# Optimization experiments

Measured on AMD Instinct MI355X. Metric: run time of the kernel, lower is better.

Reference implementation:

```python
import jax, jax.numpy as jnp
import numpy as np

E, C, FE, FS, K = 8, 1024, 1024, 4096, 2  # n_experts, embed, expert_inter, shared_inter, top_k
B, T = 4, 2048

def setup_inputs() -> dict:
    key = jax.random.key(0)
    ks = jax.random.split(key, 8)
    def init(k, shape, fan_in):
        return jax.random.normal(k, shape, jnp.float32) / np.sqrt(fan_in).astype(np.float32)
    return dict(
        x=jax.random.normal(ks[0], (B, T, C), jnp.float32),
        gate_w=init(ks[1], (E, C), C),        # nn.Linear(C, E, bias=False).weight
        ew1=init(ks[2], (E, C, FE), C),       # per-expert ln1 weights (transposed)
        ew2=init(ks[3], (E, C, FE), C),       # per-expert ln2 weights
        ewp=init(ks[4], (E, FE, C), FE),      # per-expert proj weights
        sw1=init(ks[5], (C, FS), C),          # shared FFN ln1
        sw2=init(ks[6], (C, FS), C),          # shared FFN ln2
        swp=init(ks[7], (FS, C), FS),         # shared FFN proj
    )

def reference(x, gate_w, ew1, ew2, ewp, sw1, sw2, swp):
    Bd, Td, Cd = x.shape
    xf = x.reshape(-1, Cd)                               # [N, C]
    scores = xf @ gate_w.T                               # [N, E] (eval mode: no noise)
    probs = jax.nn.softmax(scores, axis=-1)
    weights, indices = jax.lax.top_k(probs, K)           # [N, K]
    N = xf.shape[0]
    # combine[n, e] = routing weight of expert e for token n (0 if not selected)
    combine = jnp.zeros((N, E), xf.dtype).at[jnp.arange(N)[:, None], indices].add(weights)
    y = jnp.zeros_like(xf)
    for i in range(E):  # fixed small expert count; masked-dense replaces torch gather/scatter
        h = jax.nn.silu(xf @ ew1[i]) * (xf @ ew2[i])     # [N, FE] SwiGLU
        y = y + (h @ ewp[i]) * combine[:, i:i + 1]
    z = (jax.nn.silu(xf @ sw1) * (xf @ sw2)) @ swp       # shared expert (dropout p=0)
    return (y + z).reshape(Bd, Td, Cd), scores
```

## Files before the change

### kernel.cpp

```cpp
#include <hip/hip_runtime.h>

typedef unsigned short u16;
typedef unsigned int u32;
typedef __bf16 bf16x8 __attribute__((ext_vector_type(8)));
typedef float f32x4 __attribute__((ext_vector_type(4)));
typedef u16 u16x8 __attribute__((ext_vector_type(8)));

#define NTOK 8192
#define CDIM 1024
#define NEXP 8
#define FEDIM 1024
#define FSDIM 4096

#define GLD16(gp, lp) __builtin_amdgcn_global_load_lds( \
    (const __attribute__((address_space(1))) void*)(gp), \
    (__attribute__((address_space(3))) void*)(lp), 16, 0, 0)

__device__ __forceinline__ u16 f2bf(float f) {
  u32 u = __float_as_uint(f);
  u += 0x7FFFu + ((u >> 16) & 1u);
  return (u16)(u >> 16);
}
__device__ __forceinline__ float bf2f(u16 h) {
  return __uint_as_float(((u32)h) << 16);
}

__global__ __launch_bounds__(256) void gate_kernel(
    const float* __restrict__ x, const float* __restrict__ gw,
    float* __restrict__ scores, u16* __restrict__ xb, int* __restrict__ cnt,
    int* __restrict__ tok, float* __restrict__ wgt)
{
  __shared__ int lcnt[NEXP];
  __shared__ int lbase[NEXP];
  __shared__ int rec_i[32];
  __shared__ int rec_p1[32], rec_p2[32];
  __shared__ float rec_w1[32], rec_w2[32];

  int tid = threadIdx.x, wave = tid >> 6, lane = tid & 63;
  if (tid < NEXP) lcnt[tid] = 0;
  __syncthreads();

  int tbase = blockIdx.x * 32 + wave * 8;
#pragma unroll
  for (int it = 0; it < 8; ++it) {
    int n = tbase + it;
    const float4* xr = (const float4*)(x + (size_t)n * CDIM) + lane * 4;
    float4 xv[4];
#pragma unroll
    for (int j = 0; j < 4; j++) xv[j] = xr[j];
    u16x8 rA, rB;
    rA[0]=f2bf(xv[0].x); rA[1]=f2bf(xv[0].y); rA[2]=f2bf(xv[0].z); rA[3]=f2bf(xv[0].w);
    rA[4]=f2bf(xv[1].x); rA[5]=f2bf(xv[1].y); rA[6]=f2bf(xv[1].z); rA[7]=f2bf(xv[1].w);
    rB[0]=f2bf(xv[2].x); rB[1]=f2bf(xv[2].y); rB[2]=f2bf(xv[2].z); rB[3]=f2bf(xv[2].w);
    rB[4]=f2bf(xv[3].x); rB[5]=f2bf(xv[3].y); rB[6]=f2bf(xv[3].z); rB[7]=f2bf(xv[3].w);
    u16* xrow = xb + (size_t)n * CDIM + lane * 16;
    *(u16x8*)xrow = rA;
    *(u16x8*)(xrow + 8) = rB;

    float s[NEXP];
#pragma unroll
    for (int e = 0; e < NEXP; e++) {
      const float4* g = (const float4*)(gw + (size_t)e * CDIM) + lane * 4;
      float a = 0.f;
#pragma unroll
      for (int j = 0; j < 4; j++) {
        float4 gv = g[j];
        a += xv[j].x * gv.x + xv[j].y * gv.y + xv[j].z * gv.z + xv[j].w * gv.w;
      }
#pragma unroll
      for (int o = 32; o > 0; o >>= 1) a += __shfl_xor(a, o);
      s[e] = a;
    }
    if (lane == 0) {
      float m = s[0];
      for (int e = 1; e < NEXP; e++) m = fmaxf(m, s[e]);
      float p[NEXP], sum = 0.f;
      for (int e = 0; e < NEXP; e++) { p[e] = __expf(s[e] - m); sum += p[e]; }
      int i1 = 0;
      for (int e = 1; e < NEXP; e++) if (p[e] > p[i1]) i1 = e;
      int i2 = (i1 == 0) ? 1 : 0;
      for (int e = 0; e < NEXP; e++) if (e != i1 && p[e] > p[i2]) i2 = e;
      float w1 = p[i1] / sum, w2 = p[i2] / sum;
#pragma unroll
      for (int e = 0; e < NEXP; e++) scores[(size_t)n * NEXP + e] = s[e];
      int p1 = atomicAdd(&lcnt[i1], 1);
      int p2 = atomicAdd(&lcnt[i2], 1);
      int slot = wave * 8 + it;
      rec_i[slot] = i1 | (i2 << 8);
      rec_p1[slot] = p1; rec_p2[slot] = p2;
      rec_w1[slot] = w1; rec_w2[slot] = w2;
    }
  }
  __syncthreads();
  if (tid < NEXP) lbase[tid] = atomicAdd(&cnt[tid], lcnt[tid]);
  __syncthreads();
  if (tid < 32) {
    int n = blockIdx.x * 32 + tid;
    int i1 = rec_i[tid] & 0xff, i2 = rec_i[tid] >> 8;
    int q1 = lbase[i1] + rec_p1[tid];
    int q2 = lbase[i2] + rec_p2[tid];
    tok[i1 * NTOK + q1] = n; wgt[i1 * NTOK + q1] = rec_w1[tid];
    tok[i2 * NTOK + q2] = n; wgt[i2 * NTOK + q2] = rec_w2[tid];
  }
}

__global__ __launch_bounds__(256) void transpose64_kernel(
    const float* __restrict__ s0, const float* __restrict__ s1,
    const float* __restrict__ s2, u16* __restrict__ dst,
    int R, int C, int nz_per_src)
{
  __shared__ float tile[64][33];
  int z = blockIdx.z;
  int si = z / nz_per_src;
  const float* src = (si == 0) ? s0 : ((si == 1) ? s1 : s2);
  size_t sbase = (size_t)(z % nz_per_src) * R * C;
  size_t dbase = (size_t)z * R * C;
  int c0 = blockIdx.x * 32, r0 = blockIdx.y * 64;
  int tx = threadIdx.x & 31, ty = threadIdx.x >> 5;
#pragma unroll
  for (int p = 0; p < 8; p++) {
    int r = ty + p * 8;
    tile[r][tx] = src[sbase + (size_t)(r0 + r) * C + c0 + tx];
  }
  __syncthreads();
#pragma unroll
  for (int p = 0; p < 4; p++) {
    int cc = ty + p * 8;
    u32 v = (u32)f2bf(tile[2 * tx][cc]) | ((u32)f2bf(tile[2 * tx + 1][cc]) << 16);
    *(u32*)&dst[dbase + (size_t)(c0 + cc) * R + r0 + 2 * tx] = v;
  }
}

#define BM 128
#define BN 128
#define BK 32
#define TILE (BM * BK)

template<int AMODE>
__global__ __launch_bounds__(256, 2) void gemm_swiglu(
    const u16* __restrict__ A, int lda,
    const u16* __restrict__ B1, const u16* __restrict__ B2,
    size_t bstride, int ldb,
    int M, int K,
    u16* __restrict__ H, int ldh,
    const int* __restrict__ cnt, const int* __restrict__ tok)
{
  int e = blockIdx.z;
  int Mloc = (AMODE == 0) ? M : cnt[e];
  int mbase = blockIdx.y * BM;
  if (AMODE != 0 && mbase >= Mloc) return;
  int nbase = blockIdx.x * BN;
  int tid = threadIdx.x, wid = tid >> 6, lane = tid & 63;

  __shared__ __align__(16) u16 As[2][TILE];
  __shared__ __align__(16) u16 Bs1[2][TILE];
  __shared__ __align__(16) u16 Bs2[2][TILE];

  int sr = lane >> 2;
  int kg = (lane & 3) * 8;
  int arow0 = wid * 32 + sr;
  int arow1 = arow0 + 16;

  int pfx = 0;
  if (AMODE != 0) for (int i = 0; i < NEXP; i++) pfx += (i < e) ? cnt[i] : 0;

  size_t r0, r1;
  if (AMODE == 0) {
    r0 = mbase + arow0; r1 = mbase + arow1;
  } else {
    r0 = tok[e * NTOK + min(mbase + arow0, Mloc - 1)];
    r1 = tok[e * NTOK + min(mbase + arow1, Mloc - 1)];
  }
  const u16* Ap0 = A + r0 * (size_t)lda + kg;
  const u16* Ap1 = A + r1 * (size_t)lda + kg;
  size_t boff = (AMODE != 0) ? (size_t)e * bstride : 0;
  const u16* B1p0 = B1 + boff + (size_t)(nbase + arow0) * ldb + kg;
  const u16* B1p1 = B1 + boff + (size_t)(nbase + arow1) * ldb + kg;
  const u16* B2p0 = B2 + boff + (size_t)(nbase + arow0) * ldb + kg;
  const u16* B2p1 = B2 + boff + (size_t)(nbase + arow1) * ldb + kg;

  int ldsw0 = (wid * 32) * BK;
  int ldsw1 = (wid * 32 + 16) * BK;

  int wr = wid >> 1, wc = wid & 1;
  int fr = lane & 15, fgk = (lane >> 4) * 8;

  f32x4 acc1[4][4] = {};
  f32x4 acc2[4][4] = {};

  int nt = K / BK;
  GLD16(Ap0,  &As [0][ldsw0]); GLD16(Ap1,  &As [0][ldsw1]);
  GLD16(B1p0, &Bs1[0][ldsw0]); GLD16(B1p1, &Bs1[0][ldsw1]);
  GLD16(B2p0, &Bs2[0][ldsw0]); GLD16(B2p1, &Bs2[0][ldsw1]);
  Ap0 += BK; Ap1 += BK; B1p0 += BK; B1p1 += BK; B2p0 += BK; B2p1 += BK;
  __syncthreads();

  int cur = 0;
  for (int t = 0; t < nt; ++t) {
    int nxt = cur ^ 1;
    if (t + 1 < nt) {
      GLD16(Ap0,  &As [nxt][ldsw0]); GLD16(Ap1,  &As [nxt][ldsw1]);
      GLD16(B1p0, &Bs1[nxt][ldsw0]); GLD16(B1p1, &Bs1[nxt][ldsw1]);
      GLD16(B2p0, &Bs2[nxt][ldsw0]); GLD16(B2p1, &Bs2[nxt][ldsw1]);
      Ap0 += BK; Ap1 += BK; B1p0 += BK; B1p1 += BK; B2p0 += BK; B2p1 += BK;
    }
    const u16* as = As[cur];
    const u16* b1s = Bs1[cur];
    const u16* b2s = Bs2[cur];
    bf16x8 af[4], b1f[4], b2f[4];
#pragma unroll
    for (int m = 0; m < 4; m++)
      af[m] = *(const bf16x8*)&as[(wr * 64 + m * 16 + fr) * BK + fgk];
#pragma unroll
    for (int n = 0; n < 4; n++) {
      b1f[n] = *(const bf16x8*)&b1s[(wc * 64 + n * 16 + fr) * BK + fgk];
      b2f[n] = *(const bf16x8*)&b2s[(wc * 64 + n * 16 + fr) * BK + fgk];
    }
#pragma unroll
    for (int m = 0; m < 4; m++)
#pragma unroll
      for (int n = 0; n < 4; n++) {
        acc1[m][n] = __builtin_amdgcn_mfma_f32_16x16x32_bf16(af[m], b1f[n], acc1[m][n], 0, 0, 0);
        acc2[m][n] = __builtin_amdgcn_mfma_f32_16x16x32_bf16(af[m], b2f[n], acc2[m][n], 0, 0, 0);
      }
    __syncthreads();
    cur = nxt;
  }

  int fg4 = (lane >> 4) * 4;
#pragma unroll
  for (int m = 0; m < 4; m++) {
#pragma unroll
    for (int j = 0; j < 4; j++) {
      int rloc = wr * 64 + m * 16 + fg4 + j;
      int rr = mbase + rloc;
      if (AMODE != 0 && rr >= Mloc) continue;
      size_t orow = (size_t)(pfx + rr);
#pragma unroll
      for (int n = 0; n < 4; n++) {
        int col = nbase + wc * 64 + n * 16 + fr;
        float g = acc1[m][n][j];
        float v = acc2[m][n][j];
        float hv = (g / (1.f + __expf(-g))) * v;
        H[orow * (size_t)ldh + col] = f2bf(hv);
      }
    }
  }
}

template<int EPI, int AMODE>
__global__ __launch_bounds__(256, 2) void gemm_proj(
    const u16* __restrict__ A, int lda,
    const u16* __restrict__ B, size_t bstride, int ldb,
    int M, int K,
    float* __restrict__ outF, int ldo,
    const int* __restrict__ cnt, const int* __restrict__ tok,
    const float* __restrict__ wgt)
{
  int e = blockIdx.z;
  int Mloc = (AMODE == 0) ? M : cnt[e];
  int mbase = blockIdx.y * BM;
  if (AMODE != 0 && mbase >= Mloc) return;
  int nbase = blockIdx.x * BN;
  int tid = threadIdx.x, wid = tid >> 6, lane = tid & 63;

  __shared__ __align__(16) u16 As[2][TILE];
  __shared__ __align__(16) u16 Bs[2][TILE];

  int sr = lane >> 2;
  int kg = (lane & 3) * 8;
  int arow0 = wid * 32 + sr;
  int arow1 = arow0 + 16;

  int pfx = 0;
  if (AMODE != 0) for (int i = 0; i < NEXP; i++) pfx += (i < e) ? cnt[i] : 0;

  size_t r0, r1;
  if (AMODE == 0) {
    r0 = mbase + arow0; r1 = mbase + arow1;
  } else {
    r0 = pfx + min(mbase + arow0, Mloc - 1);
    r1 = pfx + min(mbase + arow1, Mloc - 1);
  }
  const u16* Ap0 = A + r0 * (size_t)lda + kg;
  const u16* Ap1 = A + r1 * (size_t)lda + kg;
  const u16* Bb = B + ((AMODE != 0) ? (size_t)e * bstride : 0);
  const u16* Bp0 = Bb + (size_t)(nbase + arow0) * ldb + kg;
  const u16* Bp1 = Bb + (size_t)(nbase + arow1) * ldb + kg;

  int ldsw0 = (wid * 32) * BK;
  int ldsw1 = (wid * 32 + 16) * BK;

  int wr = wid >> 1, wc = wid & 1;
  int fr = lane & 15, fgk = (lane >> 4) * 8;

  f32x4 acc[4][4] = {};

  int nt = K / BK;
  GLD16(Ap0, &As[0][ldsw0]); GLD16(Ap1, &As[0][ldsw1]);
  GLD16(Bp0, &Bs[0][ldsw0]); GLD16(Bp1, &Bs[0][ldsw1]);
  Ap0 += BK; Ap1 += BK; Bp0 += BK; Bp1 += BK;
  __syncthreads();

  int cur = 0;
  for (int t = 0; t < nt; ++t) {
    int nxt = cur ^ 1;
    if (t + 1 < nt) {
      GLD16(Ap0, &As[nxt][ldsw0]); GLD16(Ap1, &As[nxt][ldsw1]);
      GLD16(Bp0, &Bs[nxt][ldsw0]); GLD16(Bp1, &Bs[nxt][ldsw1]);
      Ap0 += BK; Ap1 += BK; Bp0 += BK; Bp1 += BK;
    }
    const u16* as = As[cur];
    const u16* bs = Bs[cur];
    bf16x8 af[4], bfr[4];
#pragma unroll
    for (int m = 0; m < 4; m++)
      af[m] = *(const bf16x8*)&as[(wr * 64 + m * 16 + fr) * BK + fgk];
#pragma unroll
    for (int n = 0; n < 4; n++)
      bfr[n] = *(const bf16x8*)&bs[(wc * 64 + n * 16 + fr) * BK + fgk];
#pragma unroll
    for (int m = 0; m < 4; m++)
#pragma unroll
      for (int n = 0; n < 4; n++)
        acc[m][n] = __builtin_amdgcn_mfma_f32_16x16x32_bf16(af[m], bfr[n], acc[m][n], 0, 0, 0);
    __syncthreads();
    cur = nxt;
  }

  int fg4 = (lane >> 4) * 4;
#pragma unroll
  for (int m = 0; m < 4; m++) {
#pragma unroll
    for (int j = 0; j < 4; j++) {
      int rloc = wr * 64 + m * 16 + fg4 + j;
      int rr = mbase + rloc;
      if (AMODE != 0 && rr >= Mloc) continue;
      int t = 0; float wv = 0.f;
      if (EPI == 4) { t = tok[e * NTOK + rr]; wv = wgt[e * NTOK + rr]; }
#pragma unroll
      for (int n = 0; n < 4; n++) {
        int col = nbase + wc * 64 + n * 16 + fr;
        float v = acc[m][n][j];
        if (EPI == 2) {
          outF[(size_t)rr * ldo + col] = v;
        } else {
          unsafeAtomicAdd(&outF[(size_t)t * ldo + col], v * wv);
        }
      }
    }
  }
}

extern "C" void kernel_launch(void* const* d_in, const int* in_sizes, int n_in,
                              void* d_out, int out_size, void* d_ws, size_t ws_size,
                              hipStream_t stream)
{
  const float* x   = (const float*)d_in[0];
  const float* gw  = (const float*)d_in[1];
  const float* ew1 = (const float*)d_in[2];
  const float* ew2 = (const float*)d_in[3];
  const float* ewp = (const float*)d_in[4];
  const float* sw1 = (const float*)d_in[5];
  const float* sw2 = (const float*)d_in[6];
  const float* swp = (const float*)d_in[7];
  float* out    = (float*)d_out;
  float* scores = out + (size_t)NTOK * CDIM;

  char* wsp = (char*)d_ws;
  size_t off = 0;
  auto alloc = [&](size_t bytes) -> void* {
    void* p = wsp + off; off += (bytes + 255) & ~(size_t)255; return p;
  };
  u16* xb   = (u16*)alloc((size_t)NTOK * CDIM * 2);
  u16* eall = (u16*)alloc((size_t)24 * CDIM * FEDIM * 2);
  u16* ew1t = eall;
  u16* ew2t = eall + (size_t)8 * CDIM * FEDIM;
  u16* ewpt = eall + (size_t)16 * CDIM * FEDIM;
  u16* s12t = (u16*)alloc((size_t)2 * FSDIM * CDIM * 2);
  u16* sw1t = s12t;
  u16* sw2t = s12t + (size_t)FSDIM * CDIM;
  u16* swpt = (u16*)alloc((size_t)CDIM * FSDIM * 2);
  u16* hs   = (u16*)alloc((size_t)NTOK * FSDIM * 2);
  u16* he   = hs;
  int* cnt  = (int*)alloc(256);
  int* tok  = (int*)alloc((size_t)NEXP * NTOK * 4);
  float* wgt = (float*)alloc((size_t)NEXP * NTOK * 4);
  if (off > ws_size) return;

  hipMemsetAsync(cnt, 0, 32, stream);
  gate_kernel<<<NTOK / 32, 256, 0, stream>>>(x, gw, scores, xb, cnt, tok, wgt);

  transpose64_kernel<<<dim3(FEDIM/32, CDIM/64, 24), 256, 0, stream>>>(
      ew1, ew2, ewp, eall, CDIM, FEDIM, 8);
  transpose64_kernel<<<dim3(FSDIM/32, CDIM/64, 2), 256, 0, stream>>>(
      sw1, sw2, sw1, s12t, CDIM, FSDIM, 1);
  transpose64_kernel<<<dim3(CDIM/32, FSDIM/64, 1), 256, 0, stream>>>(
      swp, swp, swp, swpt, FSDIM, CDIM, 1);

  gemm_swiglu<0><<<dim3(FSDIM/BN, NTOK/BM, 1), 256, 0, stream>>>(
      xb, CDIM, sw1t, sw2t, 0, CDIM, NTOK, CDIM, hs, FSDIM, nullptr, nullptr);
  gemm_proj<2,0><<<dim3(CDIM/BN, NTOK/BM, 1), 256, 0, stream>>>(
      hs, FSDIM, swpt, 0, FSDIM, NTOK, FSDIM, out, CDIM, nullptr, nullptr, nullptr);

  size_t estride = (size_t)FEDIM * CDIM;
  gemm_swiglu<1><<<dim3(FEDIM/BN, NTOK/BM, NEXP), 256, 0, stream>>>(
      xb, CDIM, ew1t, ew2t, estride, CDIM, 0, CDIM, he, FEDIM, cnt, tok);
  gemm_proj<4,2><<<dim3(CDIM/BN, NTOK/BM, NEXP), 256, 0, stream>>>(
      he, FEDIM, ewpt, estride, FEDIM, 0, FEDIM, out, CDIM, cnt, tok, wgt);
}
```

Before: 565.1 us.

## Merge gate/transposes, shared+expert SwiGLU, and projections into single launches

Folds the gate kernel and the three weight transposes into one prep kernel, and merges the shared and routed-expert SwiGLU GEMMs into one launch and both projection GEMMs into another, each with a flattened block index. Putting shared and expert work in the same grid lets expert blocks fill the tail of the shared GEMM and removes launch gaps. The shared projection now atomically adds into an output zeroed by a memset instead of storing directly, which adds atomic traffic and a full output memset. The expert hidden buffer gets its own allocation because both GEMMs now run concurrently.

```diff
diff --git a/kernel.cpp b/kernel.cpp
--- a/kernel.cpp
+++ b/kernel.cpp
@@ -21,15 +21,60 @@
   u += 0x7FFFu + ((u >> 16) & 1u);
   return (u16)(u >> 16);
 }
-__device__ __forceinline__ float bf2f(u16 h) {
-  return __uint_as_float(((u32)h) << 16);
-}
-
-__global__ __launch_bounds__(256) void gate_kernel(
+
+__device__ __forceinline__ void transpose64_body(
+    const float* __restrict__ src, u16* __restrict__ dst,
+    int R, int C, int bx, int by)
+{
+  __shared__ float tile[64][33];
+  int c0 = bx * 32, r0 = by * 64;
+  int tx = threadIdx.x & 31, ty = threadIdx.x >> 5;
+#pragma unroll
+  for (int p = 0; p < 8; p++) {
+    int r = ty + p * 8;
+    tile[r][tx] = src[(size_t)(r0 + r) * C + c0 + tx];
+  }
+  __syncthreads();
+#pragma unroll
+  for (int p = 0; p < 4; p++) {
+    int cc = ty + p * 8;
+    u32 v = (u32)f2bf(tile[2 * tx][cc]) | ((u32)f2bf(tile[2 * tx + 1][cc]) << 16);
+    *(u32*)&dst[(size_t)(c0 + cc) * R + r0 + 2 * tx] = v;
+  }
+}
+
+__global__ __launch_bounds__(256) void prep_kernel(
     const float* __restrict__ x, const float* __restrict__ gw,
+    const float* __restrict__ ew1, const float* __restrict__ ew2,
+    const float* __restrict__ ewp, const float* __restrict__ sw1,
+    const float* __restrict__ sw2, const float* __restrict__ swp,
     float* __restrict__ scores, u16* __restrict__ xb, int* __restrict__ cnt,
-    int* __restrict__ tok, float* __restrict__ wgt)
+    int* __restrict__ tok, float* __restrict__ wgt,
+    u16* __restrict__ eall, u16* __restrict__ s12t, u16* __restrict__ swpt)
 {
+  int bid = blockIdx.x;
+  if (bid < 12288) {
+    int z = bid >> 9, r = bid & 511;
+    const float* src = (z < 8) ? ew1 : ((z < 16) ? ew2 : ewp);
+    transpose64_body(src + (size_t)(z & 7) * CDIM * FEDIM,
+                     eall + (size_t)z * CDIM * FEDIM,
+                     CDIM, FEDIM, r & 31, r >> 5);
+    return;
+  }
+  if (bid < 16384) {
+    int i2 = bid - 12288;
+    int z = i2 >> 11, r = i2 & 2047;
+    transpose64_body(z ? sw2 : sw1, s12t + (size_t)z * CDIM * FSDIM,
+                     CDIM, FSDIM, r & 127, r >> 7);
+    return;
+  }
+  if (bid < 18432) {
+    int r = bid - 16384;
+    transpose64_body(swp, swpt, FSDIM, CDIM, r & 31, r >> 5);
+    return;
+  }
+
+  int gb = bid - 18432;
   __shared__ int lcnt[NEXP];
   __shared__ int lbase[NEXP];
   __shared__ int rec_i[32];
@@ -40,7 +85,7 @@
   if (tid < NEXP) lcnt[tid] = 0;
   __syncthreads();
 
-  int tbase = blockIdx.x * 32 + wave * 8;
+  int tbase = gb * 32 + wave * 8;
 #pragma unroll
   for (int it = 0; it < 8; ++it) {
     int n = tbase + it;
@@ -95,7 +140,7 @@
   if (tid < NEXP) lbase[tid] = atomicAdd(&cnt[tid], lcnt[tid]);
   __syncthreads();
   if (tid < 32) {
-    int n = blockIdx.x * 32 + tid;
+    int n = gb * 32 + tid;
     int i1 = rec_i[tid] & 0xff, i2 = rec_i[tid] >> 8;
     int q1 = lbase[i1] + rec_p1[tid];
     int q2 = lbase[i2] + rec_p2[tid];
@@ -104,52 +149,36 @@
   }
 }
 
-__global__ __launch_bounds__(256) void transpose64_kernel(
-    const float* __restrict__ s0, const float* __restrict__ s1,
-    const float* __restrict__ s2, u16* __restrict__ dst,
-    int R, int C, int nz_per_src)
-{
-  __shared__ float tile[64][33];
-  int z = blockIdx.z;
-  int si = z / nz_per_src;
-  const float* src = (si == 0) ? s0 : ((si == 1) ? s1 : s2);
-  size_t sbase = (size_t)(z % nz_per_src) * R * C;
-  size_t dbase = (size_t)z * R * C;
-  int c0 = blockIdx.x * 32, r0 = blockIdx.y * 64;
-  int tx = threadIdx.x & 31, ty = threadIdx.x >> 5;
-#pragma unroll
-  for (int p = 0; p < 8; p++) {
-    int r = ty + p * 8;
-    tile[r][tx] = src[sbase + (size_t)(r0 + r) * C + c0 + tx];
-  }
-  __syncthreads();
-#pragma unroll
-  for (int p = 0; p < 4; p++) {
-    int cc = ty + p * 8;
-    u32 v = (u32)f2bf(tile[2 * tx][cc]) | ((u32)f2bf(tile[2 * tx + 1][cc]) << 16);
-    *(u32*)&dst[dbase + (size_t)(c0 + cc) * R + r0 + 2 * tx] = v;
-  }
-}
-
 #define BM 128
 #define BN 128
 #define BK 32
 #define TILE (BM * BK)
 
-template<int AMODE>
-__global__ __launch_bounds__(256, 2) void gemm_swiglu(
-    const u16* __restrict__ A, int lda,
-    const u16* __restrict__ B1, const u16* __restrict__ B2,
-    size_t bstride, int ldb,
-    int M, int K,
-    u16* __restrict__ H, int ldh,
-    const int* __restrict__ cnt, const int* __restrict__ tok)
+__global__ __launch_bounds__(256, 2) void swiglu_merged(
+    const u16* __restrict__ xb,
+    const u16* __restrict__ sw1t, const u16* __restrict__ sw2t,
+    const u16* __restrict__ ew1t, const u16* __restrict__ ew2t,
+    const int* __restrict__ cnt, const int* __restrict__ tok,
+    u16* __restrict__ hs, u16* __restrict__ he)
 {
-  int e = blockIdx.z;
-  int Mloc = (AMODE == 0) ? M : cnt[e];
-  int mbase = blockIdx.y * BM;
-  if (AMODE != 0 && mbase >= Mloc) return;
-  int nbase = blockIdx.x * BN;
+  int bid = blockIdx.x;
+  bool gather; int e = 0, xB, yB, Mloc, ldh, pfx = 0;
+  const u16 *B1, *B2; u16* H;
+  if (bid < 2048) {
+    gather = false; xB = bid & 31; yB = bid >> 5;
+    Mloc = NTOK; B1 = sw1t; B2 = sw2t; H = hs; ldh = FSDIM;
+  } else {
+    int eb = bid - 2048; e = eb >> 9; int r = eb & 511;
+    xB = r & 7; yB = r >> 3;
+    gather = true;
+    Mloc = cnt[e];
+    if (yB * BM >= Mloc) return;
+    size_t es = (size_t)FEDIM * CDIM;
+    B1 = ew1t + (size_t)e * es; B2 = ew2t + (size_t)e * es;
+    H = he; ldh = FEDIM;
+    for (int i = 0; i < e; i++) pfx += cnt[i];
+  }
+  int mbase = yB * BM, nbase = xB * BN;
   int tid = threadIdx.x, wid = tid >> 6, lane = tid & 63;
 
   __shared__ __align__(16) u16 As[2][TILE];
@@ -161,23 +190,19 @@
   int arow0 = wid * 32 + sr;
   int arow1 = arow0 + 16;
 
-  int pfx = 0;
-  if (AMODE != 0) for (int i = 0; i < NEXP; i++) pfx += (i < e) ? cnt[i] : 0;
-
   size_t r0, r1;
-  if (AMODE == 0) {
+  if (!gather) {
     r0 = mbase + arow0; r1 = mbase + arow1;
   } else {
     r0 = tok[e * NTOK + min(mbase + arow0, Mloc - 1)];
     r1 = tok[e * NTOK + min(mbase + arow1, Mloc - 1)];
   }
-  const u16* Ap0 = A + r0 * (size_t)lda + kg;
-  const u16* Ap1 = A + r1 * (size_t)lda + kg;
-  size_t boff = (AMODE != 0) ? (size_t)e * bstride : 0;
-  const u16* B1p0 = B1 + boff + (size_t)(nbase + arow0) * ldb + kg;
-  const u16* B1p1 = B1 + boff + (size_t)(nbase + arow1) * ldb + kg;
-  const u16* B2p0 = B2 + boff + (size_t)(nbase + arow0) * ldb + kg;
-  const u16* B2p1 = B2 + boff + (size_t)(nbase + arow1) * ldb + kg;
+  const u16* Ap0 = xb + r0 * (size_t)CDIM + kg;
+  const u16* Ap1 = xb + r1 * (size_t)CDIM + kg;
+  const u16* B1p0 = B1 + (size_t)(nbase + arow0) * CDIM + kg;
+  const u16* B1p1 = B1 + (size_t)(nbase + arow1) * CDIM + kg;
+  const u16* B2p0 = B2 + (size_t)(nbase + arow0) * CDIM + kg;
+  const u16* B2p1 = B2 + (size_t)(nbase + arow1) * CDIM + kg;
 
   int ldsw0 = (wid * 32) * BK;
   int ldsw1 = (wid * 32 + 16) * BK;
@@ -188,7 +213,7 @@
   f32x4 acc1[4][4] = {};
   f32x4 acc2[4][4] = {};
 
-  int nt = K / BK;
+  constexpr int nt = CDIM / BK;
   GLD16(Ap0,  &As [0][ldsw0]); GLD16(Ap1,  &As [0][ldsw1]);
   GLD16(B1p0, &Bs1[0][ldsw0]); GLD16(B1p1, &Bs1[0][ldsw1]);
   GLD16(B2p0, &Bs2[0][ldsw0]); GLD16(B2p1, &Bs2[0][ldsw1]);
@@ -234,7 +259,7 @@
     for (int j = 0; j < 4; j++) {
       int rloc = wr * 64 + m * 16 + fg4 + j;
       int rr = mbase + rloc;
-      if (AMODE != 0 && rr >= Mloc) continue;
+      if (gather && rr >= Mloc) continue;
       size_t orow = (size_t)(pfx + rr);
 #pragma unroll
       for (int n = 0; n < 4; n++) {
@@ -248,20 +273,30 @@
   }
 }
 
-template<int EPI, int AMODE>
-__global__ __launch_bounds__(256, 2) void gemm_proj(
-    const u16* __restrict__ A, int lda,
-    const u16* __restrict__ B, size_t bstride, int ldb,
-    int M, int K,
-    float* __restrict__ outF, int ldo,
+__global__ __launch_bounds__(256, 2) void proj_merged(
+    const u16* __restrict__ hs, const u16* __restrict__ he,
+    const u16* __restrict__ swpt, const u16* __restrict__ ewpt,
     const int* __restrict__ cnt, const int* __restrict__ tok,
-    const float* __restrict__ wgt)
+    const float* __restrict__ wgt, float* __restrict__ out)
 {
-  int e = blockIdx.z;
-  int Mloc = (AMODE == 0) ? M : cnt[e];
-  int mbase = blockIdx.y * BM;
-  if (AMODE != 0 && mbase >= Mloc) return;
-  int nbase = blockIdx.x * BN;
+  int bid = blockIdx.x;
+  bool ex; int e = 0, xB, yB, Mloc, K, lda, pfx = 0;
+  const u16 *A, *B;
+  if (bid < 512) {
+    ex = false; xB = bid & 7; yB = bid >> 3;
+    Mloc = NTOK; K = FSDIM; lda = FSDIM; A = hs; B = swpt;
+  } else {
+    int eb = bid - 512; e = eb >> 9; int r = eb & 511;
+    xB = r & 7; yB = r >> 3;
+    ex = true;
+    Mloc = cnt[e];
+    if (yB * BM >= Mloc) return;
+    K = FEDIM; lda = FEDIM; A = he;
+    B = ewpt + (size_t)e * FEDIM * CDIM;
+    for (int i = 0; i < e; i++) pfx += cnt[i];
+  }
+  int mbase = yB * BM, nbase = xB * BN;
+  int ldb = K;
   int tid = threadIdx.x, wid = tid >> 6, lane = tid & 63;
 
   __shared__ __align__(16) u16 As[2][TILE];
@@ -272,11 +307,8 @@
   int arow0 = wid * 32 + sr;
   int arow1 = arow0 + 16;
 
-  int pfx = 0;
-  if (AMODE != 0) for (int i = 0; i < NEXP; i++) pfx += (i < e) ? cnt[i] : 0;
-
   size_t r0, r1;
-  if (AMODE == 0) {
+  if (!ex) {
     r0 = mbase + arow0; r1 = mbase + arow1;
   } else {
     r0 = pfx + min(mbase + arow0, Mloc - 1);
@@ -284,9 +316,8 @@
   }
   const u16* Ap0 = A + r0 * (size_t)lda + kg;
   const u16* Ap1 = A + r1 * (size_t)lda + kg;
-  const u16* Bb = B + ((AMODE != 0) ? (size_t)e * bstride : 0);
-  const u16* Bp0 = Bb + (size_t)(nbase + arow0) * ldb + kg;
-  const u16* Bp1 = Bb + (size_t)(nbase + arow1) * ldb + kg;
+  const u16* Bp0 = B + (size_t)(nbase + arow0) * ldb + kg;
+  const u16* Bp1 = B + (size_t)(nbase + arow1) * ldb + kg;
 
   int ldsw0 = (wid * 32) * BK;
   int ldsw1 = (wid * 32 + 16) * BK;
@@ -335,18 +366,14 @@
     for (int j = 0; j < 4; j++) {
       int rloc = wr * 64 + m * 16 + fg4 + j;
       int rr = mbase + rloc;
-      if (AMODE != 0 && rr >= Mloc) continue;
-      int t = 0; float wv = 0.f;
-      if (EPI == 4) { t = tok[e * NTOK + rr]; wv = wgt[e * NTOK + rr]; }
+      if (ex && rr >= Mloc) continue;
+      int trow; float wv;
+      if (ex) { trow = tok[e * NTOK + rr]; wv = wgt[e * NTOK + rr]; }
+      else    { trow = rr;                 wv = 1.f; }
 #pragma unroll
       for (int n = 0; n < 4; n++) {
         int col = nbase + wc * 64 + n * 16 + fr;
-        float v = acc[m][n][j];
-        if (EPI == 2) {
-          outF[(size_t)rr * ldo + col] = v;
-        } else {
-          unsafeAtomicAdd(&outF[(size_t)t * ldo + col], v * wv);
-        }
+        unsafeAtomicAdd(&out[(size_t)trow * CDIM + col], acc[m][n][j] * wv);
       }
     }
   }
@@ -382,30 +409,22 @@
   u16* sw2t = s12t + (size_t)FSDIM * CDIM;
   u16* swpt = (u16*)alloc((size_t)CDIM * FSDIM * 2);
   u16* hs   = (u16*)alloc((size_t)NTOK * FSDIM * 2);
-  u16* he   = hs;
+  u16* he   = (u16*)alloc((size_t)2 * NTOK * FEDIM * 2);
   int* cnt  = (int*)alloc(256);
   int* tok  = (int*)alloc((size_t)NEXP * NTOK * 4);
   float* wgt = (float*)alloc((size_t)NEXP * NTOK * 4);
   if (off > ws_size) return;
 
   hipMemsetAsync(cnt, 0, 32, stream);
-  gate_kernel<<<NTOK / 32, 256, 0, stream>>>(x, gw, scores, xb, cnt, tok, wgt);
-
-  transpose64_kernel<<<dim3(FEDIM/32, CDIM/64, 24), 256, 0, stream>>>(
-      ew1, ew2, ewp, eall, CDIM, FEDIM, 8);
-  transpose64_kernel<<<dim3(FSDIM/32, CDIM/64, 2), 256, 0, stream>>>(
-      sw1, sw2, sw1, s12t, CDIM, FSDIM, 1);
-  transpose64_kernel<<<dim3(CDIM/32, FSDIM/64, 1), 256, 0, stream>>>(
-      swp, swp, swp, swpt, FSDIM, CDIM, 1);
-
-  gemm_swiglu<0><<<dim3(FSDIM/BN, NTOK/BM, 1), 256, 0, stream>>>(
-      xb, CDIM, sw1t, sw2t, 0, CDIM, NTOK, CDIM, hs, FSDIM, nullptr, nullptr);
-  gemm_proj<2,0><<<dim3(CDIM/BN, NTOK/BM, 1), 256, 0, stream>>>(
-      hs, FSDIM, swpt, 0, FSDIM, NTOK, FSDIM, out, CDIM, nullptr, nullptr, nullptr);
-
-  size_t estride = (size_t)FEDIM * CDIM;
-  gemm_swiglu<1><<<dim3(FEDIM/BN, NTOK/BM, NEXP), 256, 0, stream>>>(
-      xb, CDIM, ew1t, ew2t, estride, CDIM, 0, CDIM, he, FEDIM, cnt, tok);
-  gemm_proj<4,2><<<dim3(CDIM/BN, NTOK/BM, NEXP), 256, 0, stream>>>(
-      he, FEDIM, ewpt, estride, FEDIM, 0, FEDIM, out, CDIM, cnt, tok, wgt);
-}
+  hipMemsetAsync(out, 0, (size_t)NTOK * CDIM * 4, stream);
+
+  prep_kernel<<<18688, 256, 0, stream>>>(x, gw, ew1, ew2, ewp, sw1, sw2, swp,
+                                         scores, xb, cnt, tok, wgt,
+                                         eall, s12t, swpt);
+
+  swiglu_merged<<<2048 + 4096, 256, 0, stream>>>(
+      xb, sw1t, sw2t, ew1t, ew2t, cnt, tok, hs, he);
+
+  proj_merged<<<512 + 4096, 256, 0, stream>>>(
+      hs, he, swpt, ewpt, cnt, tok, wgt, out);
+}
```

New measurement: 617.7 us. +9.3%, slower.
